# Performance work log

Measured on AMD Instinct MI355X. Metric: run time of the kernel, lower is better.

The kernel has to match this reference:

```python
import jax, jax.numpy as jnp
import numpy as np

N_NODES = 50000
N_EDGES = 400000
IN_DIM = 512
OUT_DIM = 512


def setup_inputs() -> dict:
    key = jax.random.key(0)
    k1, k2, k3, k4 = jax.random.split(key, 4)
    x = jax.random.normal(k1, (N_NODES, IN_DIM), dtype=jnp.float32)
    edge_index = jax.random.randint(k2, (2, N_EDGES), 0, N_NODES, dtype=jnp.int64)
    # nn.Linear(in_dim, out_dim): weight [out, in], bias [out]
    W = jax.random.normal(k3, (OUT_DIM, IN_DIM), dtype=jnp.float32) / np.sqrt(IN_DIM)
    b = jax.random.normal(k4, (OUT_DIM,), dtype=jnp.float32) * 0.01
    return {"x": x, "edge_index": edge_index, "W": W, "b": b}


def reference(x, edge_index, W, b):
    n = x.shape[0]
    loops = jnp.arange(n, dtype=edge_index.dtype)
    row = jnp.concatenate([edge_index[0], loops])  # src
    col = jnp.concatenate([edge_index[1], loops])  # dst
    # degree from row counts (matches torch.bincount(row)); self-loops ensure deg >= 1
    deg = jax.ops.segment_sum(jnp.ones(row.shape[0], dtype=x.dtype), row, num_segments=n)
    dis = jax.lax.rsqrt(deg)  # deg^-0.5
    norm = dis[row] * dis[col]  # [E+N]
    h = x @ W.T + b  # [N, out_dim]
    # out[dst] += norm * h[src], fused gather-scale-scatter
    out = jax.ops.segment_sum(norm[:, None] * h[row], col, num_segments=n)
    return jax.nn.relu(out)
```

## Files before the change

kernel.cpp:

```cpp
#include <hip/hip_runtime.h>
#include <hip/hip_bf16.h>

#define K_DIM 512
#define N_DIM 512

typedef __attribute__((ext_vector_type(8))) short s8v;
typedef __attribute__((ext_vector_type(4))) short s4v;
typedef __attribute__((ext_vector_type(4))) float f4v;

__device__ __forceinline__ short f2bf(float f) {
  union { float f; unsigned u; } v; v.f = f;
  unsigned r = (v.u + 0x7FFFu + ((v.u >> 16) & 1u)) >> 16;
  return (short)r;
}
__device__ __forceinline__ float bflo(unsigned u) {
  union { unsigned u; float f; } v; v.u = u << 16; return v.f;
}
__device__ __forceinline__ float bfhi(unsigned u) {
  union { unsigned u; float f; } v; v.u = u & 0xffff0000u; return v.f;
}

__device__ __forceinline__ void gload16(const void* g, void* l) {
  __builtin_amdgcn_global_load_lds(
      (const __attribute__((address_space(1))) void*)g,
      (__attribute__((address_space(3))) void*)l, 16, 0, 0);
}

__device__ __forceinline__ int edge_stride(const int* __restrict__ e32, int lane) {
  int chk = e32[2 * lane + 1];
  unsigned long long m = __ballot(chk == 0);
  return (m == ~0ULL) ? 2 : 1;
}

__global__ __launch_bounds__(256) void k_pre1(const float* __restrict__ W,
    short* __restrict__ Wb, const float* __restrict__ x, short* __restrict__ xs,
    long long totalx, const int* __restrict__ e32, int* __restrict__ outdeg,
    int* __restrict__ indeg, int E, int nbw, int nbx) {
  int b = blockIdx.x;
  int t = threadIdx.x;
  if (b < nbw) {
    int i = (b * 256 + t) * 4;
    float4 f = *(const float4*)(W + i);
    s4v s; s[0] = f2bf(f.x); s[1] = f2bf(f.y); s[2] = f2bf(f.z); s[3] = f2bf(f.w);
    *(s4v*)(Wb + i) = s;
  } else if (b < nbw + nbx) {
    long long i = ((long long)(b - nbw) * 256 + t) * 8;
    if (i < totalx) {
      float4 f0 = *(const float4*)(x + i);
      float4 f1 = *(const float4*)(x + i + 4);
      s8v v;
      v[0] = f2bf(f0.x); v[1] = f2bf(f0.y); v[2] = f2bf(f0.z); v[3] = f2bf(f0.w);
      v[4] = f2bf(f1.x); v[5] = f2bf(f1.y); v[6] = f2bf(f1.z); v[7] = f2bf(f1.w);
      *(s8v*)(xs + i) = v;
    }
  } else {
    int st = edge_stride(e32, t & 63);
    int i = (b - nbw - nbx) * 256 + t;
    if (i < E) {
      int r = e32[(size_t)i * st];
      int c = e32[(size_t)(E + i) * st];
      atomicAdd(&outdeg[r], 1);
      atomicAdd(&indeg[c], 1);
    }
  }
}

__global__ __launch_bounds__(256) void k_pre2(const int* __restrict__ outdeg,
    float* __restrict__ dis, const int* __restrict__ indeg, int* __restrict__ part,
    int n, int nbd) {
  int b = blockIdx.x;
  if (b < nbd) {
    int i = b * 256 + threadIdx.x;
    if (i < n) dis[i] = rsqrtf((float)(outdeg[i] + 1));
  } else {
    __shared__ int sm[256];
    int lb = b - nbd;
    int i = lb * 256 + threadIdx.x;
    sm[threadIdx.x] = (i < n) ? indeg[i] : 0;
    __syncthreads();
    for (int off = 128; off > 0; off >>= 1) {
      if (threadIdx.x < off) sm[threadIdx.x] += sm[threadIdx.x + off];
      __syncthreads();
    }
    if (threadIdx.x == 0) part[lb] = sm[0];
  }
}

__global__ __launch_bounds__(256) void k_scan(const int* __restrict__ indeg,
    const int* __restrict__ part, int* __restrict__ row_start,
    int* __restrict__ cursor, int n, int nb) {
  __shared__ int sp[256];
  __shared__ int sm[256];
  int t = threadIdx.x, b = blockIdx.x;
  sp[t] = (t < nb) ? part[t] : 0;
  __syncthreads();
  for (int off = 1; off < 256; off <<= 1) {
    int a = (t >= off) ? sp[t - off] : 0;
    __syncthreads();
    sp[t] += a;
    __syncthreads();
  }
  int pOff = (b > 0) ? sp[b - 1] : 0;
  if (b == 0 && t == 255) row_start[n] = sp[255];
  int i = b * 256 + t;
  int v = (i < n) ? indeg[i] : 0;
  sm[t] = v;
  __syncthreads();
  for (int off = 1; off < 256; off <<= 1) {
    int a = (t >= off) ? sm[t - off] : 0;
    __syncthreads();
    sm[t] += a;
    __syncthreads();
  }
  if (i < n) {
    int excl = pOff + sm[t] - v;
    row_start[i] = excl;
    cursor[i] = excl;
  }
}

__global__ __launch_bounds__(256) void k_fill(const int* __restrict__ e32,
    int* __restrict__ cursor, int* __restrict__ csr, int E) {
  int st = edge_stride(e32, threadIdx.x & 63);
  int i = blockIdx.x * blockDim.x + threadIdx.x;
  if (i >= E) return;
  int r = e32[(size_t)i * st];
  int c = e32[(size_t)(E + i) * st];
  int p = atomicAdd(&cursor[c], 1);
  csr[p] = r;
}

__device__ __forceinline__ void fma8(float* acc, uint4 rv, float w) {
  acc[0] += w * bflo(rv.x); acc[1] += w * bfhi(rv.x);
  acc[2] += w * bflo(rv.y); acc[3] += w * bfhi(rv.y);
  acc[4] += w * bflo(rv.z); acc[5] += w * bfhi(rv.z);
  acc[6] += w * bflo(rv.w); acc[7] += w * bfhi(rv.w);
}

__global__ __launch_bounds__(256) void k_agg(const short* __restrict__ xs,
    const float* __restrict__ dis, const int* __restrict__ row_start,
    const int* __restrict__ csr, short* __restrict__ xa, float* __restrict__ s,
    int n) {
  int wid = blockIdx.x * 4 + (threadIdx.x >> 6);
  int nw = gridDim.x * 4;
  int lane = threadIdx.x & 63;
  const short* hl = xs + lane * 8;
  for (int v = wid; v < n; v += nw) {
    float dv = dis[v];
    float acc[8];
    float accs = dv;
    {
      uint4 r = *(const uint4*)(hl + (size_t)v * N_DIM);
      acc[0] = dv * bflo(r.x); acc[1] = dv * bfhi(r.x);
      acc[2] = dv * bflo(r.y); acc[3] = dv * bfhi(r.y);
      acc[4] = dv * bflo(r.z); acc[5] = dv * bfhi(r.z);
      acc[6] = dv * bflo(r.w); acc[7] = dv * bfhi(r.w);
    }
    int sb = __builtin_amdgcn_readfirstlane(row_start[v]);
    int eb = __builtin_amdgcn_readfirstlane(row_start[v + 1]);
    int idx = sb;
    for (; idx + 8 <= eb; idx += 8) {
      int s0 = csr[idx],     s1 = csr[idx + 1], s2 = csr[idx + 2], s3 = csr[idx + 3];
      int s4 = csr[idx + 4], s5 = csr[idx + 5], s6 = csr[idx + 6], s7 = csr[idx + 7];
      float w0 = dis[s0], w1 = dis[s1], w2 = dis[s2], w3 = dis[s3];
      float w4 = dis[s4], w5 = dis[s5], w6 = dis[s6], w7 = dis[s7];
      uint4 r0 = *(const uint4*)(hl + (size_t)s0 * N_DIM);
      uint4 r1 = *(const uint4*)(hl + (size_t)s1 * N_DIM);
      uint4 r2 = *(const uint4*)(hl + (size_t)s2 * N_DIM);
      uint4 r3 = *(const uint4*)(hl + (size_t)s3 * N_DIM);
      uint4 r4 = *(const uint4*)(hl + (size_t)s4 * N_DIM);
      uint4 r5 = *(const uint4*)(hl + (size_t)s5 * N_DIM);
      uint4 r6 = *(const uint4*)(hl + (size_t)s6 * N_DIM);
      uint4 r7 = *(const uint4*)(hl + (size_t)s7 * N_DIM);
      accs += w0 + w1 + w2 + w3 + w4 + w5 + w6 + w7;
      fma8(acc, r0, w0); fma8(acc, r1, w1); fma8(acc, r2, w2); fma8(acc, r3, w3);
      fma8(acc, r4, w4); fma8(acc, r5, w5); fma8(acc, r6, w6); fma8(acc, r7, w7);
    }
    for (; idx + 4 <= eb; idx += 4) {
      int s0 = csr[idx], s1 = csr[idx + 1], s2 = csr[idx + 2], s3 = csr[idx + 3];
      float w0 = dis[s0], w1 = dis[s1], w2 = dis[s2], w3 = dis[s3];
      uint4 r0 = *(const uint4*)(hl + (size_t)s0 * N_DIM);
      uint4 r1 = *(const uint4*)(hl + (size_t)s1 * N_DIM);
      uint4 r2 = *(const uint4*)(hl + (size_t)s2 * N_DIM);
      uint4 r3 = *(const uint4*)(hl + (size_t)s3 * N_DIM);
      accs += w0 + w1 + w2 + w3;
      fma8(acc, r0, w0); fma8(acc, r1, w1); fma8(acc, r2, w2); fma8(acc, r3, w3);
    }
    for (; idx < eb; ++idx) {
      int s0 = csr[idx];
      float w0 = dis[s0];
      uint4 r0 = *(const uint4*)(hl + (size_t)s0 * N_DIM);
      accs += w0;
      fma8(acc, r0, w0);
    }
    s8v o;
    #pragma unroll
    for (int q = 0; q < 8; ++q) o[q] = f2bf(dv * acc[q]);
    *(s8v*)(xa + (size_t)v * N_DIM + lane * 8) = o;
    if (lane == 0) s[v] = dv * accs;
  }
}

__global__ __launch_bounds__(256, 4) void k_gemm(const short* __restrict__ xa,
    const short* __restrict__ Wb, const float* __restrict__ bias,
    const float* __restrict__ s, float* __restrict__ out, int M) {
  __shared__ __align__(16) char smem[32768];
  short* As = (short*)smem;
  short* Bs = (short*)(smem + 16384);
  int nwg = gridDim.x;
  int orig = blockIdx.x;
  int q8 = nwg >> 3, r8 = nwg & 7;
  int xcd = orig & 7, pos = orig >> 3;
  int swz = (xcd < r8 ? xcd * (q8 + 1) : r8 * (q8 + 1) + (xcd - r8) * q8) + pos;
  const int n0 = (swz & 3) * 128;
  const int m0 = (swz >> 2) * 128;

  const int tid = threadIdx.x;
  const int lane = tid & 63;
  const int wv = tid >> 6, wr = wv >> 1, wc = wv & 1;
  const int la = lane & 15, lg = lane >> 4;

  const short* ag[2];
  const short* bg[2];
  int doff[2];
  #pragma unroll
  for (int r = 0; r < 2; ++r) {
    int id = r * 256 + tid;
    int row = id >> 2;
    int ch = id & 3;
    int arow = m0 + row; if (arow >= M) arow = M - 1;
    ag[r] = xa + (size_t)arow * K_DIM + ch * 8;
    bg[r] = Wb + (size_t)(n0 + row) * K_DIM + ch * 8;
    doff[r] = (r * 256 + (tid & 192)) * 16;
  }
  int aro[4], bro[4];
  #pragma unroll
  for (int i = 0; i < 4; ++i) {
    aro[i] = (64 * wr + 16 * i + la) * 64 + lg * 16;
    bro[i] = (64 * wc + 16 * i + la) * 64 + lg * 16;
  }

  f4v acc[4][4] = {};

  #pragma unroll
  for (int r = 0; r < 2; ++r) {
    gload16(ag[r], (char*)As + doff[r]);
    gload16(bg[r], (char*)Bs + doff[r]);
  }
  __syncthreads();

  for (int kt = 0; kt < 16; ++kt) {
    const int cur = kt & 1;
    const int nxt = cur ^ 1;
    if (kt < 15) {
      const int kk = (kt + 1) * 32;
      #pragma unroll
      for (int r = 0; r < 2; ++r) {
        gload16(ag[r] + kk, (char*)As + nxt * 8192 + doff[r]);
        gload16(bg[r] + kk, (char*)Bs + nxt * 8192 + doff[r]);
      }
    }
    s8v af[4], bf[4];
    const char* ab = (const char*)As + cur * 8192;
    const char* bb = (const char*)Bs + cur * 8192;
    #pragma unroll
    for (int i = 0; i < 4; ++i) af[i] = *(const s8v*)(ab + aro[i]);
    #pragma unroll
    for (int j = 0; j < 4; ++j) bf[j] = *(const s8v*)(bb + bro[j]);
    #pragma unroll
    for (int i = 0; i < 4; ++i)
      #pragma unroll
      for (int j = 0; j < 4; ++j)
        acc[i][j] = __builtin_amdgcn_mfma_f32_16x16x32_bf16(af[i], bf[j], acc[i][j], 0, 0, 0);
    __syncthreads();
  }

  float* Es = (float*)(smem + wv * 4352);
  float bv[4];
  #pragma unroll
  for (int j = 0; j < 4; ++j) bv[j] = bias[n0 + 64 * wc + 16 * j + la];
  #pragma unroll
  for (int i = 0; i < 4; ++i) {
    int rowb = m0 + 64 * wr + 16 * i + lg * 4;
    float sv[4];
    #pragma unroll
    for (int r = 0; r < 4; ++r) sv[r] = (rowb + r < M) ? s[rowb + r] : 0.f;
    #pragma unroll
    for (int j = 0; j < 4; ++j)
      #pragma unroll
      for (int r = 0; r < 4; ++r)
        Es[(lg * 4 + r) * 68 + 16 * j + la] = fmaxf(acc[i][j][r] + sv[r] * bv[j], 0.f);
    asm volatile("s_waitcnt lgkmcnt(0)" ::: "memory");
    int gr0 = m0 + 64 * wr + 16 * i;
    #pragma unroll
    for (int rr = 0; rr < 4; ++rr) {
      int id = rr * 64 + lane;
      int rl = id >> 4, ch = id & 15;
      f4v val = *(const f4v*)&Es[rl * 68 + ch * 4];
      if (gr0 + rl < M)
        __builtin_nontemporal_store(val,
            (f4v*)(out + (size_t)(gr0 + rl) * N_DIM + n0 + 64 * wc + ch * 4));
    }
    asm volatile("s_waitcnt lgkmcnt(0)" ::: "memory");
  }
}

extern "C" void kernel_launch(void* const* d_in, const int* in_sizes, int n_in,
                              void* d_out, int out_size, void* d_ws, size_t ws_size,
                              hipStream_t stream) {
  const float* x = (const float*)d_in[0];
  const int* e32 = (const int*)d_in[1];
  const float* W = (const float*)d_in[2];
  const float* bias = (const float*)d_in[3];
  float* out = (float*)d_out;
  int M = in_sizes[0] / K_DIM;
  int E = in_sizes[1] / 2;

  char* ws = (char*)d_ws;
  size_t off = 0;
  auto alloc = [&](size_t bytes) {
    void* p = ws + off;
    off = (off + bytes + 255) & ~(size_t)255;
    return p;
  };
  short* Wb      = (short*)alloc((size_t)N_DIM * K_DIM * 2);
  short* xa      = (short*)alloc((size_t)M * N_DIM * 2);
  float* dis     = (float*)alloc((size_t)M * 4);
  float* sv      = (float*)alloc((size_t)M * 4);
  int*   outdeg  = (int*)alloc((size_t)M * 4);
  int*   indeg   = (int*)alloc((size_t)M * 4);
  int*   rstart  = (int*)alloc((size_t)(M + 1) * 4);
  int*   cursor  = (int*)alloc((size_t)M * 4);
  int*   part    = (int*)alloc(256 * 4);
  int*   csr     = (int*)alloc((size_t)E * 4);
  if (off > ws_size) return;

  short* xs = (short*)d_out;

  size_t zbytes = (size_t)((char*)indeg - (char*)outdeg) + (size_t)M * 4;
  (void)hipMemsetAsync(outdeg, 0, zbytes, stream);

  long long totalx = (long long)M * K_DIM;
  int nbw = N_DIM * K_DIM / 4 / 256;
  int nbx = (int)((totalx / 8 + 255) / 256);
  int nbh = (E + 255) / 256;
  k_pre1<<<nbw + nbx + nbh, 256, 0, stream>>>(W, Wb, x, xs, totalx, e32,
                                              outdeg, indeg, E, nbw, nbx);
  int nscan = (M + 255) / 256;
  k_pre2<<<nscan * 2, 256, 0, stream>>>(outdeg, dis, indeg, part, M, nscan);
  k_scan<<<nscan, 256, 0, stream>>>(indeg, part, rstart, cursor, M, nscan);
  k_fill<<<nbh, 256, 0, stream>>>(e32, cursor, csr, E);
  k_agg<<<2048, 256, 0, stream>>>(xs, dis, rstart, csr, xa, sv, M);
  int nmc = (M + 127) / 128;
  k_gemm<<<nmc * 4, 256, 0, stream>>>(xa, Wb, bias, sv, out, M);
}
```

Baseline: 204.0 us.

## Merge degree/partial kernels into scan and triple-buffer GEMM K loop

Drops the k_pre2 kernel. k_scan now computes dis itself and gets each block's prefix offset by redundantly summing all earlier indeg entries, which removes one launch at the cost of quadratic redundant reads. The GEMM main loop moves from double to triple buffering in 48KB of LDS, with loads issued two stages ahead and explicit vmcnt waits plus barriers. Occupancy drops from 4 to 3 workgroups per CU in exchange for deeper prefetch.

```diff
diff --git a/kernel.cpp b/kernel.cpp
--- a/kernel.cpp
+++ b/kernel.cpp
@@ -65,44 +65,23 @@
   }
 }
 
-__global__ __launch_bounds__(256) void k_pre2(const int* __restrict__ outdeg,
-    float* __restrict__ dis, const int* __restrict__ indeg, int* __restrict__ part,
-    int n, int nbd) {
-  int b = blockIdx.x;
-  if (b < nbd) {
-    int i = b * 256 + threadIdx.x;
-    if (i < n) dis[i] = rsqrtf((float)(outdeg[i] + 1));
-  } else {
-    __shared__ int sm[256];
-    int lb = b - nbd;
-    int i = lb * 256 + threadIdx.x;
-    sm[threadIdx.x] = (i < n) ? indeg[i] : 0;
-    __syncthreads();
-    for (int off = 128; off > 0; off >>= 1) {
-      if (threadIdx.x < off) sm[threadIdx.x] += sm[threadIdx.x + off];
-      __syncthreads();
-    }
-    if (threadIdx.x == 0) part[lb] = sm[0];
-  }
-}
-
 __global__ __launch_bounds__(256) void k_scan(const int* __restrict__ indeg,
-    const int* __restrict__ part, int* __restrict__ row_start,
-    int* __restrict__ cursor, int n, int nb) {
-  __shared__ int sp[256];
+    const int* __restrict__ outdeg, float* __restrict__ dis,
+    int* __restrict__ row_start, int* __restrict__ cursor, int n) {
   __shared__ int sm[256];
   int t = threadIdx.x, b = blockIdx.x;
-  sp[t] = (t < nb) ? part[t] : 0;
+  int i = b * 256 + t;
+  if (i < n) dis[i] = rsqrtf((float)(outdeg[i] + 1));
+  int base = 0;
+  for (int j = t; j < b * 256; j += 256) base += indeg[j];
+  sm[t] = base;
   __syncthreads();
-  for (int off = 1; off < 256; off <<= 1) {
-    int a = (t >= off) ? sp[t - off] : 0;
+  for (int off = 128; off > 0; off >>= 1) {
+    if (t < off) sm[t] += sm[t + off];
     __syncthreads();
-    sp[t] += a;
-    __syncthreads();
-  }
-  int pOff = (b > 0) ? sp[b - 1] : 0;
-  if (b == 0 && t == 255) row_start[n] = sp[255];
-  int i = b * 256 + t;
+  }
+  int pOff = sm[0];
+  __syncthreads();
   int v = (i < n) ? indeg[i] : 0;
   sm[t] = v;
   __syncthreads();
@@ -117,6 +96,7 @@
     row_start[i] = excl;
     cursor[i] = excl;
   }
+  if (b == gridDim.x - 1 && t == 255) row_start[n] = pOff + sm[255];
 }
 
 __global__ __launch_bounds__(256) void k_fill(const int* __restrict__ e32,
@@ -201,12 +181,10 @@
   }
 }
 
-__global__ __launch_bounds__(256, 4) void k_gemm(const short* __restrict__ xa,
+__global__ __launch_bounds__(256, 3) void k_gemm(const short* __restrict__ xa,
     const short* __restrict__ Wb, const float* __restrict__ bias,
     const float* __restrict__ s, float* __restrict__ out, int M) {
-  __shared__ __align__(16) char smem[32768];
-  short* As = (short*)smem;
-  short* Bs = (short*)(smem + 16384);
+  __shared__ __align__(16) char smem[49152];
   int nwg = gridDim.x;
   int orig = blockIdx.x;
   int q8 = nwg >> 3, r8 = nwg & 7;
@@ -242,38 +220,45 @@
 
   f4v acc[4][4] = {};
 
-  #pragma unroll
-  for (int r = 0; r < 2; ++r) {
-    gload16(ag[r], (char*)As + doff[r]);
-    gload16(bg[r], (char*)Bs + doff[r]);
-  }
+#define STAGE(TT) do {                                                  \
+    const int kkk = (TT) * 32;                                          \
+    char* bufp = smem + ((TT) % 3) * 16384;                             \
+    gload16(ag[0] + kkk, bufp + doff[0]);                               \
+    gload16(ag[1] + kkk, bufp + doff[1]);                               \
+    gload16(bg[0] + kkk, bufp + 8192 + doff[0]);                        \
+    gload16(bg[1] + kkk, bufp + 8192 + doff[1]);                        \
+  } while (0)
+
+#define STEP(TT, VMC) do {                                              \
+    if ((TT) + 2 < 16) STAGE((TT) + 2);                                 \
+    asm volatile("s_waitcnt vmcnt(" #VMC ")\n\ts_barrier" ::: "memory"); \
+    __builtin_amdgcn_sched_barrier(0);                                  \
+    const char* ab = (const char*)smem + ((TT) % 3) * 16384;            \
+    const char* bb = ab + 8192;                                         \
+    s8v af[4], bf[4];                                                   \
+    af[0] = *(const s8v*)(ab + aro[0]); af[1] = *(const s8v*)(ab + aro[1]); \
+    af[2] = *(const s8v*)(ab + aro[2]); af[3] = *(const s8v*)(ab + aro[3]); \
+    bf[0] = *(const s8v*)(bb + bro[0]); bf[1] = *(const s8v*)(bb + bro[1]); \
+    bf[2] = *(const s8v*)(bb + bro[2]); bf[3] = *(const s8v*)(bb + bro[3]); \
+    _Pragma("unroll")                                                   \
+    for (int i = 0; i < 4; ++i)                                         \
+      _Pragma("unroll")                                                 \
+      for (int j = 0; j < 4; ++j)                                       \
+        acc[i][j] = __builtin_amdgcn_mfma_f32_16x16x32_bf16(af[i], bf[j], acc[i][j], 0, 0, 0); \
+    __builtin_amdgcn_sched_barrier(0);                                  \
+    asm volatile("s_barrier" ::: "memory");                             \
+  } while (0)
+
+  STAGE(0);
+  STAGE(1);
+  STEP(0, 8);  STEP(1, 8);  STEP(2, 8);  STEP(3, 8);
+  STEP(4, 8);  STEP(5, 8);  STEP(6, 8);  STEP(7, 8);
+  STEP(8, 8);  STEP(9, 8);  STEP(10, 8); STEP(11, 8);
+  STEP(12, 8); STEP(13, 8); STEP(14, 4); STEP(15, 0);
+#undef STEP
+#undef STAGE
+
   __syncthreads();
-
-  for (int kt = 0; kt < 16; ++kt) {
-    const int cur = kt & 1;
-    const int nxt = cur ^ 1;
-    if (kt < 15) {
-      const int kk = (kt + 1) * 32;
-      #pragma unroll
-      for (int r = 0; r < 2; ++r) {
-        gload16(ag[r] + kk, (char*)As + nxt * 8192 + doff[r]);
-        gload16(bg[r] + kk, (char*)Bs + nxt * 8192 + doff[r]);
-      }
-    }
-    s8v af[4], bf[4];
-    const char* ab = (const char*)As + cur * 8192;
-    const char* bb = (const char*)Bs + cur * 8192;
-    #pragma unroll
-    for (int i = 0; i < 4; ++i) af[i] = *(const s8v*)(ab + aro[i]);
-    #pragma unroll
-    for (int j = 0; j < 4; ++j) bf[j] = *(const s8v*)(bb + bro[j]);
-    #pragma unroll
-    for (int i = 0; i < 4; ++i)
-      #pragma unroll
-      for (int j = 0; j < 4; ++j)
-        acc[i][j] = __builtin_amdgcn_mfma_f32_16x16x32_bf16(af[i], bf[j], acc[i][j], 0, 0, 0);
-    __syncthreads();
-  }
 
   float* Es = (float*)(smem + wv * 4352);
   float bv[4];
@@ -331,7 +316,6 @@
   int*   indeg   = (int*)alloc((size_t)M * 4);
   int*   rstart  = (int*)alloc((size_t)(M + 1) * 4);
   int*   cursor  = (int*)alloc((size_t)M * 4);
-  int*   part    = (int*)alloc(256 * 4);
   int*   csr     = (int*)alloc((size_t)E * 4);
   if (off > ws_size) return;
 
@@ -347,8 +331,7 @@
   k_pre1<<<nbw + nbx + nbh, 256, 0, stream>>>(W, Wb, x, xs, totalx, e32,
                                               outdeg, indeg, E, nbw, nbx);
   int nscan = (M + 255) / 256;
-  k_pre2<<<nscan * 2, 256, 0, stream>>>(outdeg, dis, indeg, part, M, nscan);
-  k_scan<<<nscan, 256, 0, stream>>>(indeg, part, rstart, cursor, M, nscan);
+  k_scan<<<nscan, 256, 0, stream>>>(indeg, outdeg, dis, rstart, cursor, M);
   k_fill<<<nbh, 256, 0, stream>>>(e32, cursor, csr, E);
   k_agg<<<2048, 256, 0, stream>>>(xs, dis, rstart, csr, xa, sv, M);
   int nmc = (M + 127) / 128;
```

New measurement: 226.5 us. 11.1% more time.

## Split aggregation into two column-half passes to shrink gather working set

Applied to the files above, without the earlier changes.

The neighbor aggregation kernel now processes only 256 of the 512 feature columns per launch and is run twice, once per half. Each lane loads 8 bytes instead of 16 per neighbor row. The intent is to halve the bf16 feature working set touched per pass (about 25 MB instead of 50 MB) so random row gathers hit in cache more often. The cost is reading the CSR structure and dis values twice, an extra kernel launch, and smaller per-lane loads with fewer bytes in flight.

```diff
diff --git a/kernel.cpp b/kernel.cpp
--- a/kernel.cpp
+++ b/kernel.cpp
@@ -130,31 +130,27 @@
   csr[p] = r;
 }
 
-__device__ __forceinline__ void fma8(float* acc, uint4 rv, float w) {
+__device__ __forceinline__ void fma4(float* acc, uint2 rv, float w) {
   acc[0] += w * bflo(rv.x); acc[1] += w * bfhi(rv.x);
   acc[2] += w * bflo(rv.y); acc[3] += w * bfhi(rv.y);
-  acc[4] += w * bflo(rv.z); acc[5] += w * bfhi(rv.z);
-  acc[6] += w * bflo(rv.w); acc[7] += w * bfhi(rv.w);
 }
 
 __global__ __launch_bounds__(256) void k_agg(const short* __restrict__ xs,
     const float* __restrict__ dis, const int* __restrict__ row_start,
     const int* __restrict__ csr, short* __restrict__ xa, float* __restrict__ s,
-    int n) {
+    int n, int coff, int writeS) {
   int wid = blockIdx.x * 4 + (threadIdx.x >> 6);
   int nw = gridDim.x * 4;
   int lane = threadIdx.x & 63;
-  const short* hl = xs + lane * 8;
+  const short* hl = xs + coff + lane * 4;
   for (int v = wid; v < n; v += nw) {
     float dv = dis[v];
-    float acc[8];
+    float acc[4];
     float accs = dv;
     {
-      uint4 r = *(const uint4*)(hl + (size_t)v * N_DIM);
+      uint2 r = *(const uint2*)(hl + (size_t)v * N_DIM);
       acc[0] = dv * bflo(r.x); acc[1] = dv * bfhi(r.x);
       acc[2] = dv * bflo(r.y); acc[3] = dv * bfhi(r.y);
-      acc[4] = dv * bflo(r.z); acc[5] = dv * bfhi(r.z);
-      acc[6] = dv * bflo(r.w); acc[7] = dv * bfhi(r.w);
     }
     int sb = __builtin_amdgcn_readfirstlane(row_start[v]);
     int eb = __builtin_amdgcn_readfirstlane(row_start[v + 1]);
@@ -164,40 +160,40 @@
       int s4 = csr[idx + 4], s5 = csr[idx + 5], s6 = csr[idx + 6], s7 = csr[idx + 7];
       float w0 = dis[s0], w1 = dis[s1], w2 = dis[s2], w3 = dis[s3];
       float w4 = dis[s4], w5 = dis[s5], w6 = dis[s6], w7 = dis[s7];
-      uint4 r0 = *(const uint4*)(hl + (size_t)s0 * N_DIM);
-      uint4 r1 = *(const uint4*)(hl + (size_t)s1 * N_DIM);
-      uint4 r2 = *(const uint4*)(hl + (size_t)s2 * N_DIM);
-      uint4 r3 = *(const uint4*)(hl + (size_t)s3 * N_DIM);
-      uint4 r4 = *(const uint4*)(hl + (size_t)s4 * N_DIM);
-      uint4 r5 = *(const uint4*)(hl + (size_t)s5 * N_DIM);
-      uint4 r6 = *(const uint4*)(hl + (size_t)s6 * N_DIM);
-      uint4 r7 = *(const uint4*)(hl + (size_t)s7 * N_DIM);
+      uint2 r0 = *(const uint2*)(hl + (size_t)s0 * N_DIM);
+      uint2 r1 = *(const uint2*)(hl + (size_t)s1 * N_DIM);
+      uint2 r2 = *(const uint2*)(hl + (size_t)s2 * N_DIM);
+      uint2 r3 = *(const uint2*)(hl + (size_t)s3 * N_DIM);
+      uint2 r4 = *(const uint2*)(hl + (size_t)s4 * N_DIM);
+      uint2 r5 = *(const uint2*)(hl + (size_t)s5 * N_DIM);
+      uint2 r6 = *(const uint2*)(hl + (size_t)s6 * N_DIM);
+      uint2 r7 = *(const uint2*)(hl + (size_t)s7 * N_DIM);
       accs += w0 + w1 + w2 + w3 + w4 + w5 + w6 + w7;
-      fma8(acc, r0, w0); fma8(acc, r1, w1); fma8(acc, r2, w2); fma8(acc, r3, w3);
-      fma8(acc, r4, w4); fma8(acc, r5, w5); fma8(acc, r6, w6); fma8(acc, r7, w7);
+      fma4(acc, r0, w0); fma4(acc, r1, w1); fma4(acc, r2, w2); fma4(acc, r3, w3);
+      fma4(acc, r4, w4); fma4(acc, r5, w5); fma4(acc, r6, w6); fma4(acc, r7, w7);
     }
     for (; idx + 4 <= eb; idx += 4) {
       int s0 = csr[idx], s1 = csr[idx + 1], s2 = csr[idx + 2], s3 = csr[idx + 3];
       float w0 = dis[s0], w1 = dis[s1], w2 = dis[s2], w3 = dis[s3];
-      uint4 r0 = *(const uint4*)(hl + (size_t)s0 * N_DIM);
-      uint4 r1 = *(const uint4*)(hl + (size_t)s1 * N_DIM);
-      uint4 r2 = *(const uint4*)(hl + (size_t)s2 * N_DIM);
-      uint4 r3 = *(const uint4*)(hl + (size_t)s3 * N_DIM);
+      uint2 r0 = *(const uint2*)(hl + (size_t)s0 * N_DIM);
+      uint2 r1 = *(const uint2*)(hl + (size_t)s1 * N_DIM);
+      uint2 r2 = *(const uint2*)(hl + (size_t)s2 * N_DIM);
+      uint2 r3 = *(const uint2*)(hl + (size_t)s3 * N_DIM);
       accs += w0 + w1 + w2 + w3;
-      fma8(acc, r0, w0); fma8(acc, r1, w1); fma8(acc, r2, w2); fma8(acc, r3, w3);
+      fma4(acc, r0, w0); fma4(acc, r1, w1); fma4(acc, r2, w2); fma4(acc, r3, w3);
     }
     for (; idx < eb; ++idx) {
       int s0 = csr[idx];
       float w0 = dis[s0];
-      uint4 r0 = *(const uint4*)(hl + (size_t)s0 * N_DIM);
+      uint2 r0 = *(const uint2*)(hl + (size_t)s0 * N_DIM);
       accs += w0;
-      fma8(acc, r0, w0);
-    }
-    s8v o;
-    #pragma unroll
-    for (int q = 0; q < 8; ++q) o[q] = f2bf(dv * acc[q]);
-    *(s8v*)(xa + (size_t)v * N_DIM + lane * 8) = o;
-    if (lane == 0) s[v] = dv * accs;
+      fma4(acc, r0, w0);
+    }
+    s4v o;
+    o[0] = f2bf(dv * acc[0]); o[1] = f2bf(dv * acc[1]);
+    o[2] = f2bf(dv * acc[2]); o[3] = f2bf(dv * acc[3]);
+    *(s4v*)(xa + (size_t)v * N_DIM + coff + lane * 4) = o;
+    if (writeS && lane == 0) s[v] = dv * accs;
   }
 }
 
@@ -350,7 +346,8 @@
   k_pre2<<<nscan * 2, 256, 0, stream>>>(outdeg, dis, indeg, part, M, nscan);
   k_scan<<<nscan, 256, 0, stream>>>(indeg, part, rstart, cursor, M, nscan);
   k_fill<<<nbh, 256, 0, stream>>>(e32, cursor, csr, E);
-  k_agg<<<2048, 256, 0, stream>>>(xs, dis, rstart, csr, xa, sv, M);
+  k_agg<<<2048, 256, 0, stream>>>(xs, dis, rstart, csr, xa, sv, M, 0, 1);
+  k_agg<<<2048, 256, 0, stream>>>(xs, dis, rstart, csr, xa, sv, M, 256, 0);
   int nmc = (M + 127) / 128;
   k_gemm<<<nmc * 4, 256, 0, stream>>>(xa, Wb, bias, sv, out, M);
 }
```

Result: no change. 203.0 us (-0.5%).
